# Kernel optimization log

Measured on AMD Instinct MI355X. Metric: run time of the kernel, lower is better.

## Reference

```python
import jax, jax.numpy as jnp
import numpy as np

B, C, D, T = 64, 512, 32, 32
DT = D * T
K = 128            # valid_num: top-K proposals kept for NMS-style pooling
MARGIN = 0.2       # opt.global_margin
MAX_VIOLATION = True
EPS = 1e-8         # torch.cosine_similarity eps


def _l2n(x, axis):
    # torch cosine_similarity normalizes each vector by max(||x||, eps)
    return x / jnp.maximum(jnp.linalg.norm(x, axis=axis, keepdims=True), EPS)


def _cos(a, b, axis):
    return jnp.sum(_l2n(a, axis) * _l2n(b, axis), axis=axis)


def setup_inputs() -> dict:
    key = jax.random.key(0)
    k1, k2, k3 = jax.random.split(key, 3)
    videos = jax.random.normal(k1, (B, C, D, T), jnp.float32)
    sentences = jax.random.normal(k2, (B, C), jnp.float32)
    iou = jax.random.uniform(k3, (DT, DT), jnp.float32)
    iou_maps = 0.5 * (iou + iou.T)
    iou_maps = iou_maps.at[jnp.arange(DT), jnp.arange(DT)].set(1.0)
    mask = jnp.ones((D, T), jnp.float32)
    lam = jnp.asarray(0.125, jnp.float32)
    return {"videos": videos, "sentences": sentences, "lam": lam,
            "mask": mask, "valid_num": K, "iou_maps": iou_maps}


def reference(videos, sentences, lam, mask, valid_num, iou_maps):
    b, c, d, t = videos.shape
    dt = d * t
    # center over channel dim (dim=1 in torch)
    V = videos - jnp.mean(videos, axis=1, keepdims=True)          # [b,c,d,t]
    S = sentences - jnp.mean(sentences, axis=1, keepdims=True)    # [b,c]
    Vf = V.reshape(b, c, dt)
    Vn = _l2n(Vf, axis=1)                                         # unit over c
    Sn = _l2n(S, axis=1)
    mflat = mask.reshape(dt)

    # cosine sim of every sentence vs every video proposal: [b_sent, b_vid, dt]
    cross = jnp.einsum('ic,jcp->ijp', Sn, Vn)
    cross = jnp.where(mflat == 0, -jnp.inf, cross)

    # --- per-sample positive pooling (loop 1) ---
    self_score = cross[jnp.arange(b), jnp.arange(b)]              # [b, dt]
    w = jax.nn.softmax(self_score, axis=-1)
    video_pos = jnp.einsum('bp,bcp->bc', w, Vf)                   # [b, c]

    # sentence-sentence sims + hard negative mining
    sim = Sn @ Sn.T                                               # [b, b]
    idx = jnp.argsort(-sim, axis=1)                               # descending
    neg_idx = idx[:, 6:b - 5]                                     # b > 11 path
    neg_sents = S[neg_idx]                                        # [b, b-11, c]
    pos_score = _cos(video_pos, S, axis=1)                        # [b]
    neg_score = _cos(video_pos[:, None, :], neg_sents, axis=2)    # [b, b-11]
    vas_loss = jnp.mean(jax.nn.relu(MARGIN + neg_score - pos_score[:, None]), axis=1).mean()

    # cross-video pseudo-positive (crov), gated on nearest-neighbor sim > 0.9
    nn_idx = idx[:, 1]
    pse = Vf[nn_idx]                                              # [b, c, dt]
    vsim = jax.nn.softmax(_cos(video_pos[:, :, None], pse, axis=1), axis=-1)  # [b, dt]
    p_v = jnp.einsum('bp,bcp->bc', vsim, pse)
    n_v = jnp.einsum('bp,bcp->bc', (1.0 - vsim) * mflat, pse) / (valid_num - 1)
    crov = jax.nn.relu(MARGIN + _cos(video_pos, n_v, axis=1) - _cos(video_pos, p_v, axis=1))
    gate = sim[jnp.arange(b), nn_idx] > 0.9
    crov_loss = jnp.where(gate, crov, 0.0).mean()

    # --- NMS-weighted video score pooling (loop 2) ---
    pmap = self_score.reshape(b, d, t)                            # postive_map
    topv, topi = jax.lax.top_k(cross, valid_num)                  # [b,b,K]
    # pairwise IoU among the top-K proposals of each (sentence, video) pair
    iou = iou_maps[topi[..., :, None], topi[..., None, :]]        # [b,b,K,K]
    lower = jnp.tril(jnp.ones((valid_num, valid_num), bool), -1)  # l < k
    decay = jnp.prod(1.0 - jnp.where(lower, iou, 0.0), axis=-1)   # [b,b,K]
    wk = jax.nn.softmax(lam * topv, axis=-1)
    scores = jnp.sum(wk * decay * topv, axis=-1)                  # [b,b]

    # bidirectional margin ranking loss
    diag = jnp.diag(scores)[:, None]
    eye = jnp.eye(b, dtype=bool)
    cost_s = jnp.where(eye, 0.0, jax.nn.relu(MARGIN + scores - diag))
    cost_im = jnp.where(eye, 0.0, jax.nn.relu(MARGIN + scores - diag.T))
    if MAX_VIOLATION:
        cost_s = cost_s.max(axis=1)
        cost_im = cost_im.max(axis=0)
    loss = cost_s.sum() / b + cost_im.sum() / b + vas_loss + crov_loss
    return loss, pmap
```

## Files before the change

kernel.cpp:

```cpp
#include <hip/hip_runtime.h>
#include <hip/hip_fp16.h>
#include <math.h>

#define BB 64
#define CC 512
#define DTT 1024
#define NNEG 53
#define MARGIN_ 0.2f
#define EPSV 1e-8f
#define KC 32

__device__ __forceinline__ float bred_sum(float v, float* red, int tid, int nt) {
  red[tid] = v; __syncthreads();
  for (int s = nt >> 1; s > 0; s >>= 1) { if (tid < s) red[tid] += red[tid + s]; __syncthreads(); }
  float r = red[0]; __syncthreads();
  return r;
}
__device__ __forceinline__ float bred_max(float v, float* red, int tid, int nt) {
  red[tid] = v; __syncthreads();
  for (int s = nt >> 1; s > 0; s >>= 1) { if (tid < s) red[tid] = fmaxf(red[tid], red[tid + s]); __syncthreads(); }
  float r = red[0]; __syncthreads();
  return r;
}

__global__ void k_sent(const float* __restrict__ sent, float* __restrict__ Sn,
                       float* __restrict__ SnT, float* __restrict__ SnSum) {
  int b = blockIdx.x, tid = threadIdx.x;
  __shared__ float red[256];
  float x0 = sent[b * CC + tid], x1 = sent[b * CC + tid + 256];
  float mean = bred_sum(x0 + x1, red, tid, 256) * (1.0f / CC);
  float s0 = x0 - mean, s1 = x1 - mean;
  float ss = bred_sum(s0 * s0 + s1 * s1, red, tid, 256);
  float nrm = fmaxf(sqrtf(ss), EPSV);
  float n0 = s0 / nrm, n1 = s1 / nrm;
  Sn[b * CC + tid] = n0; Sn[b * CC + tid + 256] = n1;
  SnT[tid * BB + b] = n0; SnT[(tid + 256) * BB + b] = n1;
  float sn = bred_sum(n0 + n1, red, tid, 256);
  if (tid == 0) SnSum[b] = sn;
}

__global__ void k_sim(const float* __restrict__ Sn, int* __restrict__ nn_idx,
                      int* __restrict__ negidx, float* __restrict__ nnsim) {
  int i = blockIdx.x, j = threadIdx.x;
  float dot = 0.f;
  for (int c = 0; c < CC; ++c) dot += Sn[i * CC + c] * Sn[j * CC + c];
  __shared__ float srow[BB];
  srow[j] = dot; __syncthreads();
  float mv = srow[j];
  int rank = 0;
  for (int k = 0; k < BB; ++k) {
    float vk = srow[k];
    if (vk > mv || (vk == mv && k < j)) rank++;
  }
  if (rank == 1) { nn_idx[i] = j; nnsim[i] = mv; }
  if (rank >= 6 && rank < 59) negidx[i * NNEG + rank - 6] = j;
}

__global__ void k_prep_iou(const float* __restrict__ iou, __half* __restrict__ L16) {
  int g = (blockIdx.x * 256 + threadIdx.x) * 4;
  float4 x = *(const float4*)(iou + g);
  __half2 h0 = __floats2half2_rn(1.f - x.x, 1.f - x.y);
  __half2 h1 = __floats2half2_rn(1.f - x.z, 1.f - x.w);
  *(__half2*)(L16 + g) = h0;
  *(__half2*)(L16 + g + 2) = h1;
}

__global__ __launch_bounds__(256) void k_cross(const float* __restrict__ videos,
    const float* __restrict__ SnT, const float* __restrict__ SnSum,
    const float* __restrict__ mask, float* __restrict__ cross,
    float* __restrict__ meanv, float* __restrict__ normv) {
  __shared__ float As[KC][68];
  __shared__ float Bs[KC][132];
  __shared__ float Smb[128], Sinv[128];
  int tid = threadIdx.x;
  int j = blockIdx.x >> 3;
  int p0 = (blockIdx.x & 7) << 7;
  int px = tid & 31;
  int iy = tid >> 5;
  int r = tid >> 3;
  int ca = (tid & 7) * 8;
  int cb = (tid & 7) * 16;
  const float* vrow = videos + (size_t)j * CC * DTT + p0 + cb;
  const float* arow0 = SnT + r * BB + ca;

  float acc[8][4];
#pragma unroll
  for (int a = 0; a < 8; ++a)
#pragma unroll
    for (int q = 0; q < 4; ++q) acc[a][q] = 0.f;
  float s4[4] = {0.f, 0.f, 0.f, 0.f}, ss4[4] = {0.f, 0.f, 0.f, 0.f};

  float4 a0 = *(const float4*)(arow0);
  float4 a1 = *(const float4*)(arow0 + 4);
  const float* vr0 = vrow + (size_t)r * DTT;
  float4 b0 = *(const float4*)(vr0);
  float4 b1 = *(const float4*)(vr0 + 4);
  float4 b2 = *(const float4*)(vr0 + 8);
  float4 b3 = *(const float4*)(vr0 + 12);

  for (int kc = 0; kc < CC; kc += KC) {
    *(float4*)&As[r][ca] = a0; *(float4*)&As[r][ca + 4] = a1;
    *(float4*)&Bs[r][cb] = b0; *(float4*)&Bs[r][cb + 4] = b1;
    *(float4*)&Bs[r][cb + 8] = b2; *(float4*)&Bs[r][cb + 12] = b3;
    __syncthreads();
    if (kc + KC < CC) {
      const float* ar = SnT + (size_t)(kc + KC + r) * BB + ca;
      a0 = *(const float4*)(ar); a1 = *(const float4*)(ar + 4);
      const float* vr = vrow + (size_t)(kc + KC + r) * DTT;
      b0 = *(const float4*)(vr); b1 = *(const float4*)(vr + 4);
      b2 = *(const float4*)(vr + 8); b3 = *(const float4*)(vr + 12);
    }
#pragma unroll
    for (int kk = 0; kk < KC; ++kk) {
      float bq[4], ai[8];
      *(float4*)&bq[0] = *(const float4*)&Bs[kk][px * 4];
      *(float4*)&ai[0] = *(const float4*)&As[kk][iy * 8];
      *(float4*)&ai[4] = *(const float4*)&As[kk][iy * 8 + 4];
      if (iy == 0) {
#pragma unroll
        for (int q = 0; q < 4; ++q) { s4[q] += bq[q]; ss4[q] = fmaf(bq[q], bq[q], ss4[q]); }
      }
#pragma unroll
      for (int a = 0; a < 8; ++a)
#pragma unroll
        for (int q = 0; q < 4; ++q)
          acc[a][q] = fmaf(ai[a], bq[q], acc[a][q]);
    }
    __syncthreads();
  }

  if (iy == 0) {
#pragma unroll
    for (int q = 0; q < 4; ++q) {
      float mb = s4[q] * (1.0f / CC);
      float var = ss4[q] - s4[q] * mb;
      float nrm = fmaxf(sqrtf(fmaxf(var, 0.f)), EPSV);
      meanv[j * DTT + p0 + px * 4 + q] = mb;
      normv[j * DTT + p0 + px * 4 + q] = nrm;
      Smb[px * 4 + q] = mb;
      Sinv[px * 4 + q] = 1.f / nrm;
    }
  }
  __syncthreads();
  float mb[4], inv[4], mk[4];
#pragma unroll
  for (int q = 0; q < 4; ++q) {
    mb[q] = Smb[px * 4 + q];
    inv[q] = Sinv[px * 4 + q];
    mk[q] = mask[p0 + px * 4 + q];
  }
#pragma unroll
  for (int a = 0; a < 8; ++a) {
    int i = iy * 8 + a;
    float sni = SnSum[i];
    float4 outv;
    float tmp[4];
#pragma unroll
    for (int q = 0; q < 4; ++q) {
      float val = (acc[a][q] - mb[q] * sni) * inv[q];
      tmp[q] = (mk[q] == 0.f) ? -INFINITY : val;
    }
    outv.x = tmp[0]; outv.y = tmp[1]; outv.z = tmp[2]; outv.w = tmp[3];
    *(float4*)(cross + ((size_t)i * BB + j) * DTT + p0 + px * 4) = outv;
  }
}

__global__ void k_softmax_w(const float* __restrict__ cross, const float* __restrict__ meanv,
                            float* __restrict__ pmap, float* __restrict__ w, float* __restrict__ wm) {
  int b = blockIdx.x, tid = threadIdx.x;
  __shared__ float red[256];
  const float* row = cross + ((size_t)b * BB + b) * DTT;
  float v[4]; float mx = -INFINITY;
#pragma unroll
  for (int q = 0; q < 4; ++q) {
    v[q] = row[q * 256 + tid];
    pmap[b * DTT + q * 256 + tid] = v[q];
    mx = fmaxf(mx, v[q]);
  }
  mx = bred_max(mx, red, tid, 256);
  float e[4]; float se = 0.f;
#pragma unroll
  for (int q = 0; q < 4; ++q) { e[q] = expf(v[q] - mx); se += e[q]; }
  se = bred_sum(se, red, tid, 256);
  float inv = 1.f / se;
  float wmacc = 0.f;
#pragma unroll
  for (int q = 0; q < 4; ++q) {
    float wv = e[q] * inv;
    w[b * DTT + q * 256 + tid] = wv;
    wmacc += wv * meanv[b * DTT + q * 256 + tid];
  }
  wmacc = bred_sum(wmacc, red, tid, 256);
  if (tid == 0) wm[b] = wmacc;
}

__global__ void k_vpos(const float* __restrict__ videos, const float* __restrict__ w,
                       const float* __restrict__ wm, float* __restrict__ vp) {
  int wid = (blockIdx.x * 256 + threadIdx.x) >> 6;
  int lane = threadIdx.x & 63;
  int b = wid >> 9, c = wid & 511;
  const float4* vb = (const float4*)(videos + (size_t)(b * CC + c) * DTT) + lane * 4;
  const float4* wb = (const float4*)(w + b * DTT) + lane * 4;
  float acc = 0.f;
#pragma unroll
  for (int q = 0; q < 4; ++q) {
    float4 x = vb[q], y = wb[q];
    acc += x.x * y.x + x.y * y.y + x.z * y.z + x.w * y.w;
  }
#pragma unroll
  for (int off = 32; off > 0; off >>= 1) acc += __shfl_xor(acc, off);
  if (lane == 0) vp[b * CC + c] = acc - wm[b];
}

__global__ void k_vpnorm(const float* __restrict__ vp, float* __restrict__ vpn,
                         float* __restrict__ vpsum) {
  int b = blockIdx.x, tid = threadIdx.x;
  __shared__ float red[256];
  float x0 = vp[b * CC + tid], x1 = vp[b * CC + tid + 256];
  float ss = bred_sum(x0 * x0 + x1 * x1, red, tid, 256);
  float sm = bred_sum(x0 + x1, red, tid, 256);
  if (tid == 0) { vpn[b] = fmaxf(sqrtf(ss), EPSV); vpsum[b] = sm; }
}

__global__ void k_vsim_logits(const float* __restrict__ videos, const float* __restrict__ vp,
    const float* __restrict__ vpn, const float* __restrict__ vpsum, const int* __restrict__ nn_idx,
    const float* __restrict__ meanv, const float* __restrict__ normv, float* __restrict__ vslog) {
  int gid = blockIdx.x * 256 + threadIdx.x;
  int b = gid >> 10, p = gid & 1023;
  int nn = nn_idx[b];
  const float* base = videos + (size_t)nn * CC * DTT + p;
  const float* vpr = vp + b * CC;
  float acc = 0.f;
#pragma unroll 8
  for (int c = 0; c < CC; ++c) acc = fmaf(vpr[c], base[(size_t)c * DTT], acc);
  acc -= meanv[nn * DTT + p] * vpsum[b];
  vslog[gid] = acc / (vpn[b] * normv[nn * DTT + p]);
}

__global__ void k_softmax_vsim(float* __restrict__ vslog, const int* __restrict__ nn_idx,
    const float* __restrict__ meanv, const float* __restrict__ mask,
    float* __restrict__ svp, float* __restrict__ svn) {
  int b = blockIdx.x, tid = threadIdx.x;
  __shared__ float red[256];
  int nn = nn_idx[b];
  float v[4]; float mx = -INFINITY;
#pragma unroll
  for (int q = 0; q < 4; ++q) { v[q] = vslog[b * DTT + q * 256 + tid]; mx = fmaxf(mx, v[q]); }
  mx = bred_max(mx, red, tid, 256);
  float e[4]; float se = 0.f;
#pragma unroll
  for (int q = 0; q < 4; ++q) { e[q] = expf(v[q] - mx); se += e[q]; }
  se = bred_sum(se, red, tid, 256);
  float inv = 1.f / se;
  float sp = 0.f, sn2 = 0.f;
#pragma unroll
  for (int q = 0; q < 4; ++q) {
    int p = q * 256 + tid;
    float vs = e[q] * inv;
    vslog[b * DTT + p] = vs;
    float mm = meanv[nn * DTT + p];
    sp += vs * mm;
    sn2 += (1.f - vs) * mask[p] * mm;
  }
  sp = bred_sum(sp, red, tid, 256);
  sn2 = bred_sum(sn2, red, tid, 256);
  if (tid == 0) { svp[b] = sp; svn[b] = sn2; }
}

__global__ void k_pvnv(const float* __restrict__ videos, const float* __restrict__ vsim,
    const int* __restrict__ nn_idx, const float* __restrict__ mask,
    const float* __restrict__ svp, const float* __restrict__ svn, const int* __restrict__ vn_p,
    float* __restrict__ pv, float* __restrict__ nv) {
  int wid = (blockIdx.x * 256 + threadIdx.x) >> 6;
  int lane = threadIdx.x & 63;
  int b = wid >> 9, c = wid & 511;
  int nn = nn_idx[b];
  const float4* vb = (const float4*)(videos + (size_t)(nn * CC + c) * DTT) + lane * 4;
  const float4* vs4 = (const float4*)(vsim + b * DTT) + lane * 4;
  const float4* m4 = ((const float4*)mask) + lane * 4;
  float ap = 0.f, an = 0.f;
#pragma unroll
  for (int q = 0; q < 4; ++q) {
    float4 x = vb[q], s = vs4[q], m = m4[q];
    ap += x.x * s.x + x.y * s.y + x.z * s.z + x.w * s.w;
    an += x.x * (1.f - s.x) * m.x + x.y * (1.f - s.y) * m.y + x.z * (1.f - s.z) * m.z + x.w * (1.f - s.w) * m.w;
  }
#pragma unroll
  for (int off = 32; off > 0; off >>= 1) { ap += __shfl_xor(ap, off); an += __shfl_xor(an, off); }
  if (lane == 0) {
    float kd = (float)(*vn_p - 1);
    pv[b * CC + c] = ap - svp[b];
    nv[b * CC + c] = (an - svn[b]) / kd;
  }
}

__global__ void k_vas(const float* __restrict__ vp, const float* __restrict__ vpn,
                      const float* __restrict__ Sn, const int* __restrict__ negidx,
                      float* __restrict__ vasrow) {
  int i = blockIdx.x, tid = threadIdx.x;
  __shared__ float red[64];
  __shared__ float pos;
  float invn = 1.f / vpn[i];
  float val = 0.f;
  if (tid < NNEG) {
    int nj = negidx[i * NNEG + tid];
    float d = 0.f;
    for (int c = 0; c < CC; ++c) d += vp[i * CC + c] * Sn[nj * CC + c];
    val = d * invn;
  }
  if (tid == 63) {
    float d = 0.f;
    for (int c = 0; c < CC; ++c) d += vp[i * CC + c] * Sn[i * CC + c];
    pos = d * invn;
  }
  __syncthreads();
  float contrib = (tid < NNEG) ? fmaxf(MARGIN_ + val - pos, 0.f) : 0.f;
  float s = bred_sum(contrib, red, tid, 64);
  if (tid == 0) vasrow[i] = s / (float)NNEG;
}

__global__ void k_crov(const float* __restrict__ vp, const float* __restrict__ vpn,
                       const float* __restrict__ pv, const float* __restrict__ nv,
                       const float* __restrict__ nnsim, float* __restrict__ crovrow) {
  int b = blockIdx.x, tid = threadIdx.x;
  __shared__ float red[256];
  float dp = 0.f, pp = 0.f, dn = 0.f, nn2 = 0.f;
  for (int c = tid; c < CC; c += 256) {
    float a = vp[b * CC + c], x = pv[b * CC + c], y = nv[b * CC + c];
    dp += a * x; pp += x * x; dn += a * y; nn2 += y * y;
  }
  dp = bred_sum(dp, red, tid, 256);
  pp = bred_sum(pp, red, tid, 256);
  dn = bred_sum(dn, red, tid, 256);
  nn2 = bred_sum(nn2, red, tid, 256);
  if (tid == 0) {
    float cosp = dp / (vpn[b] * fmaxf(sqrtf(pp), EPSV));
    float cosn = dn / (vpn[b] * fmaxf(sqrtf(nn2), EPSV));
    float crov = fmaxf(MARGIN_ + cosn - cosp, 0.f);
    crovrow[b] = (nnsim[b] > 0.9f) ? crov : 0.f;
  }
}

__global__ __launch_bounds__(256) void k_select(const float* __restrict__ cross,
    const int* __restrict__ vn_p, unsigned* __restrict__ ordi_g, float* __restrict__ ordv_g) {
  __shared__ unsigned int hist_s[4][256];
  __shared__ unsigned int sel_s[4][128];
  __shared__ unsigned int selk_s[4][128];
  __shared__ unsigned int cnt_s[4];
  int tid = threadIdx.x;
  int wv = tid >> 6, lane = tid & 63;
  int ij = blockIdx.x * 4 + wv;
  int K = *vn_p; if (K > 128) K = 128;
  unsigned int* hist = hist_s[wv];
  unsigned int* sel = sel_s[wv];
  unsigned int* selk = selk_s[wv];

  const float* row = cross + (size_t)ij * DTT;
  unsigned int v[16];
#pragma unroll
  for (int q = 0; q < 16; ++q) {
    unsigned u = __float_as_uint(row[q * 64 + lane]);
    v[q] = (u & 0x80000000u) ? ~u : (u | 0x80000000u);
  }
  if (lane == 0) cnt_s[wv] = 0u;
  __builtin_amdgcn_wave_barrier();

  unsigned prefix = 0u, pmask = 0u;
  int remaining = K;
  for (int shift = 24; shift >= 0; shift -= 8) {
#pragma unroll
    for (int q = 0; q < 4; ++q) hist[lane * 4 + q] = 0u;
    __builtin_amdgcn_wave_barrier();
#pragma unroll
    for (int q = 0; q < 16; ++q) {
      if ((v[q] & pmask) == prefix)
        atomicAdd(&hist[(v[q] >> shift) & 255u], 1u);
    }
    __builtin_amdgcn_wave_barrier();
    unsigned c0 = hist[lane * 4], c1 = hist[lane * 4 + 1];
    unsigned c2 = hist[lane * 4 + 2], c3 = hist[lane * 4 + 3];
    unsigned s = c0 + c1 + c2 + c3;
    unsigned inc = s;
#pragma unroll
    for (int off = 1; off < 64; off <<= 1) {
      unsigned t = __shfl_down(inc, off);
      if (lane + off < 64) inc += t;
    }
    unsigned exc = inc - s;
    bool found = (exc < (unsigned)remaining) && (inc >= (unsigned)remaining);
    unsigned long long bmask = __ballot(found);
    int winner = (int)(__ffsll((unsigned long long)bmask) - 1);
    unsigned packed = 0u;
    if (found) {
      unsigned c = exc;
      unsigned cc[4] = {c0, c1, c2, c3};
      int d = lane * 4;
#pragma unroll
      for (int q = 3; q >= 0; --q) {
        if (c + cc[q] >= (unsigned)remaining) { d = lane * 4 + q; break; }
        c += cc[q];
      }
      packed = ((unsigned)d << 16) | (unsigned)(remaining - (int)c);
    }
    packed = __shfl(packed, winner);
    prefix |= (packed >> 16) << shift;
    remaining = (int)(packed & 0xFFFFu);
    pmask |= 255u << shift;
  }

#pragma unroll
  for (int q = 0; q < 16; ++q) {
    if (v[q] > prefix) {
      unsigned pos = atomicAdd(&cnt_s[wv], 1u);
      sel[pos] = (unsigned)(q * 64 + lane);
      selk[pos] = v[q];
    }
  }
  __builtin_amdgcn_wave_barrier();
  {
    int base = K - remaining;
    int last = -1;
    for (int t = 0; t < remaining; ++t) {
      int mymin = 0x7FFFFFFF;
#pragma unroll
      for (int q = 0; q < 16; ++q) {
        int idx = q * 64 + lane;
        if (v[q] == prefix && idx > last && idx < mymin) mymin = idx;
      }
#pragma unroll
      for (int off = 32; off > 0; off >>= 1) mymin = min(mymin, __shfl_xor(mymin, off));
      if (lane == 0) { sel[base + t] = (unsigned)mymin; selk[base + t] = prefix; }
      last = mymin;
    }
  }
  __builtin_amdgcn_wave_barrier();

  for (int e = lane; e < K; e += 64) {
    unsigned myidx = sel[e], myk = selk[e];
    int rank = 0;
    for (int m = 0; m < K; ++m) {
      unsigned ok = selk[m];
      rank += (ok > myk || (ok == myk && sel[m] < myidx)) ? 1 : 0;
    }
    unsigned u = (myk & 0x80000000u) ? (myk & 0x7FFFFFFFu) : ~myk;
    ordi_g[ij * 128 + rank] = myidx;
    ordv_g[ij * 128 + rank] = __uint_as_float(u);
  }
}

__global__ __launch_bounds__(256) void k_decay(const __half* __restrict__ L16,
    const unsigned* __restrict__ ordi_g, const float* __restrict__ ordv_g,
    const float* __restrict__ lam_p, const int* __restrict__ vn_p,
    float* __restrict__ scores) {
  __shared__ unsigned ti[128];
  __shared__ float dks[128];
  int ij = blockIdx.x, tid = threadIdx.x;
  int wv = tid >> 6, lane = tid & 63;
  int K = *vn_p; if (K > 128) K = 128;
  float lam = *lam_p;
  if (tid < 128) {
    ti[tid] = (tid < K) ? ordi_g[ij * 128 + tid] : 0u;
    dks[tid] = 1.f;
  }
  __syncthreads();

  for (int r = wv; r < K; r += 4) {
    const __half* irow = L16 + (size_t)ti[r] * DTT;
    float f = 1.f;
    if (lane < r && lane < 64) f = __half2float(irow[ti[lane]]);
    float prod = f;
#pragma unroll
    for (int off = 32; off > 0; off >>= 1) prod *= __shfl_xor(prod, off);
    if (r > 64 && prod > 1e-14f) {
      float f2 = 1.f;
      int m = 64 + lane;
      if (m < r) f2 = __half2float(irow[ti[m]]);
#pragma unroll
      for (int off = 32; off > 0; off >>= 1) f2 *= __shfl_xor(f2, off);
      prod *= f2;
    }
    if (lane == 0) dks[r] = prod;
  }
  __syncthreads();

  if (wv == 0) {
    bool okA = (lane < K), okB = (lane + 64 < K);
    float vA = okA ? ordv_g[ij * 128 + lane] : 0.f;
    float vB = okB ? ordv_g[ij * 128 + lane + 64] : 0.f;
    float mx = fmaxf(okA ? lam * vA : -INFINITY, okB ? lam * vB : -INFINITY);
#pragma unroll
    for (int off = 32; off > 0; off >>= 1) mx = fmaxf(mx, __shfl_xor(mx, off));
    float eA = okA ? expf(lam * vA - mx) : 0.f;
    float eB = okB ? expf(lam * vB - mx) : 0.f;
    float se = eA + eB;
    float sc = (okA ? eA * dks[lane] * vA : 0.f) + (okB ? eB * dks[lane + 64] * vB : 0.f);
#pragma unroll
    for (int off = 32; off > 0; off >>= 1) {
      se += __shfl_xor(se, off);
      sc += __shfl_xor(sc, off);
    }
    if (lane == 0) scores[ij] = sc / se;
  }
}

__global__ void k_final(const float* __restrict__ scores, const float* __restrict__ vasrow,
                        const float* __restrict__ crovrow, float* __restrict__ out) {
  int tid = threadIdx.x;
  __shared__ float sm[BB * BB];
  __shared__ float red[64];
  for (int q = tid; q < BB * BB; q += 64) sm[q] = scores[q];
  __syncthreads();
  float di = sm[tid * BB + tid];
  float rowmax = 0.f, colmax = 0.f;
  for (int k = 0; k < BB; ++k) {
    if (k != tid) {
      rowmax = fmaxf(rowmax, fmaxf(MARGIN_ + sm[tid * BB + k] - di, 0.f));
      colmax = fmaxf(colmax, fmaxf(MARGIN_ + sm[k * BB + tid] - di, 0.f));
    }
  }
  float total = bred_sum(rowmax + colmax + vasrow[tid] + crovrow[tid], red, tid, 64);
  if (tid == 0) out[0] = total * (1.0f / BB);
}

extern "C" void kernel_launch(void* const* d_in, const int* in_sizes, int n_in,
                              void* d_out, int out_size, void* d_ws, size_t ws_size,
                              hipStream_t stream) {
  const float* videos = (const float*)d_in[0];
  const float* sentences = (const float*)d_in[1];
  const float* lam = (const float*)d_in[2];
  const float* mask = (const float*)d_in[3];
  const int* valid_num = (const int*)d_in[4];
  const float* iou_maps = (const float*)d_in[5];
  float* out = (float*)d_out;
  float* pmap = out + 1;

  float* ws = (float*)d_ws;
  float* Sn = ws;
  float* SnT = Sn + 32768;
  float* SnSum = SnT + 32768;
  float* meanv = SnSum + 64;
  float* normv = meanv + 65536;
  float* cross = normv + 65536;
  float* w = cross + 4194304;
  float* wm = w + 65536;
  float* vp = wm + 64;
  float* vpn = vp + 32768;
  float* vpsum = vpn + 64;
  float* nnsim = vpsum + 64;
  float* vslog = nnsim + 64;
  float* svp = vslog + 65536;
  float* svn = svp + 64;
  float* pvb = svn + 64;
  float* nvb = pvb + 32768;
  float* vasrow = nvb + 32768;
  float* crovrow = vasrow + 64;
  float* scores = crovrow + 64;
  int* nn_idx = (int*)(scores + 4096);
  int* negidx = nn_idx + 64;
  unsigned* ordi_g = (unsigned*)(negidx + 3392);
  float* ordv_g = (float*)(ordi_g + 524288);
  __half* L16 = (__half*)(ordv_g + 524288);

  k_sent<<<64, 256, 0, stream>>>(sentences, Sn, SnT, SnSum);
  k_sim<<<64, 64, 0, stream>>>(Sn, nn_idx, negidx, nnsim);
  k_prep_iou<<<1024, 256, 0, stream>>>(iou_maps, L16);
  k_cross<<<512, 256, 0, stream>>>(videos, SnT, SnSum, mask, cross, meanv, normv);
  k_softmax_w<<<64, 256, 0, stream>>>(cross, meanv, pmap, w, wm);
  k_vpos<<<8192, 256, 0, stream>>>(videos, w, wm, vp);
  k_vpnorm<<<64, 256, 0, stream>>>(vp, vpn, vpsum);
  k_vsim_logits<<<256, 256, 0, stream>>>(videos, vp, vpn, vpsum, nn_idx, meanv, normv, vslog);
  k_softmax_vsim<<<64, 256, 0, stream>>>(vslog, nn_idx, meanv, mask, svp, svn);
  k_pvnv<<<8192, 256, 0, stream>>>(videos, vslog, nn_idx, mask, svp, svn, valid_num, pvb, nvb);
  k_vas<<<64, 64, 0, stream>>>(vp, vpn, Sn, negidx, vasrow);
  k_crov<<<64, 256, 0, stream>>>(vp, vpn, pvb, nvb, nnsim, crovrow);
  k_select<<<1024, 256, 0, stream>>>(cross, valid_num, ordi_g, ordv_g);
  k_decay<<<4096, 256, 0, stream>>>(L16, ordi_g, ordv_g, lam, valid_num, scores);
  k_final<<<1, 64, 0, stream>>>(scores, vasrow, crovrow, out);
}
```

Before: 459.2 us.

## Compute cross similarity GEMM with split-bf16 MFMA instead of fp32 FMA

Replaces the scalar fp32 FMA tiled GEMM in k_cross with bf16 MFMA 16x16x32 instructions. It uses a three-term hi/lo bf16 split (hi*hi, hi*lo, lo*hi) so the products stay close to fp32 accuracy. Sentence vectors are pre-split into hi/lo bf16 arrays in k_sent, and video tiles are split on the fly into LDS. Channel mean and variance are reduced across threads through shared memory. This targets the FMA-bound GEMM but adds conversion work and a small precision change from the dropped lo*lo term.

```diff
diff --git a/kernel.cpp b/kernel.cpp
--- a/kernel.cpp
+++ b/kernel.cpp
@@ -8,7 +8,10 @@
 #define NNEG 53
 #define MARGIN_ 0.2f
 #define EPSV 1e-8f
-#define KC 32
+#define LDB 132
+
+typedef short s16x8 __attribute__((ext_vector_type(8)));
+typedef float f32x4 __attribute__((ext_vector_type(4)));
 
 __device__ __forceinline__ float bred_sum(float v, float* red, int tid, int nt) {
   red[tid] = v; __syncthreads();
@@ -24,7 +27,8 @@
 }
 
 __global__ void k_sent(const float* __restrict__ sent, float* __restrict__ Sn,
-                       float* __restrict__ SnT, float* __restrict__ SnSum) {
+                       unsigned short* __restrict__ SnH, unsigned short* __restrict__ SnL,
+                       float* __restrict__ SnSum) {
   int b = blockIdx.x, tid = threadIdx.x;
   __shared__ float red[256];
   float x0 = sent[b * CC + tid], x1 = sent[b * CC + tid + 256];
@@ -34,7 +38,13 @@
   float nrm = fmaxf(sqrtf(ss), EPSV);
   float n0 = s0 / nrm, n1 = s1 / nrm;
   Sn[b * CC + tid] = n0; Sn[b * CC + tid + 256] = n1;
-  SnT[tid * BB + b] = n0; SnT[(tid + 256) * BB + b] = n1;
+  unsigned u0 = __float_as_uint(n0), u1 = __float_as_uint(n1);
+  SnH[b * CC + tid] = (unsigned short)(u0 >> 16);
+  SnH[b * CC + tid + 256] = (unsigned short)(u1 >> 16);
+  float l0 = n0 - __uint_as_float(u0 & 0xFFFF0000u);
+  float l1 = n1 - __uint_as_float(u1 & 0xFFFF0000u);
+  SnL[b * CC + tid] = (unsigned short)(__float_as_uint(l0) >> 16);
+  SnL[b * CC + tid + 256] = (unsigned short)(__float_as_uint(l1) >> 16);
   float sn = bred_sum(n0 + n1, red, tid, 256);
   if (tid == 0) SnSum[b] = sn;
 }
@@ -66,102 +76,139 @@
 }
 
 __global__ __launch_bounds__(256) void k_cross(const float* __restrict__ videos,
-    const float* __restrict__ SnT, const float* __restrict__ SnSum,
-    const float* __restrict__ mask, float* __restrict__ cross,
-    float* __restrict__ meanv, float* __restrict__ normv) {
-  __shared__ float As[KC][68];
-  __shared__ float Bs[KC][132];
-  __shared__ float Smb[128], Sinv[128];
+    const unsigned short* __restrict__ SnH, const unsigned short* __restrict__ SnL,
+    const float* __restrict__ SnSum, const float* __restrict__ mask,
+    float* __restrict__ cross, float* __restrict__ meanv, float* __restrict__ normv) {
+  __shared__ unsigned int BH[16][LDB];
+  __shared__ unsigned int BL[16][LDB];
+  __shared__ float SnSum_s[64];
+  __shared__ float mb_s[128];
+  __shared__ float inv_s[128];
+
   int tid = threadIdx.x;
   int j = blockIdx.x >> 3;
   int p0 = (blockIdx.x & 7) << 7;
-  int px = tid & 31;
-  int iy = tid >> 5;
-  int r = tid >> 3;
-  int ca = (tid & 7) * 8;
-  int cb = (tid & 7) * 16;
-  const float* vrow = videos + (size_t)j * CC * DTT + p0 + cb;
-  const float* arow0 = SnT + r * BB + ca;
-
-  float acc[8][4];
-#pragma unroll
-  for (int a = 0; a < 8; ++a)
-#pragma unroll
-    for (int q = 0; q < 4; ++q) acc[a][q] = 0.f;
-  float s4[4] = {0.f, 0.f, 0.f, 0.f}, ss4[4] = {0.f, 0.f, 0.f, 0.f};
-
-  float4 a0 = *(const float4*)(arow0);
-  float4 a1 = *(const float4*)(arow0 + 4);
-  const float* vr0 = vrow + (size_t)r * DTT;
-  float4 b0 = *(const float4*)(vr0);
-  float4 b1 = *(const float4*)(vr0 + 4);
-  float4 b2 = *(const float4*)(vr0 + 8);
-  float4 b3 = *(const float4*)(vr0 + 12);
-
-  for (int kc = 0; kc < CC; kc += KC) {
-    *(float4*)&As[r][ca] = a0; *(float4*)&As[r][ca + 4] = a1;
-    *(float4*)&Bs[r][cb] = b0; *(float4*)&Bs[r][cb + 4] = b1;
-    *(float4*)&Bs[r][cb + 8] = b2; *(float4*)&Bs[r][cb + 12] = b3;
+  int lane = tid & 63;
+  int wv = tid >> 6;
+  int row = lane & 15;
+  int g = lane >> 4;
+  int g8 = g << 3;
+  int pA = wv << 5;
+
+  int kp = tid >> 4;
+  int pb = (tid & 15) << 3;
+
+  const float* vbase = videos + ((size_t)j * CC) * DTT + p0;
+
+  f32x4 acc[4][2];
+#pragma unroll
+  for (int a = 0; a < 4; ++a)
+#pragma unroll
+    for (int pf = 0; pf < 2; ++pf)
+#pragma unroll
+      for (int r = 0; r < 4; ++r) acc[a][pf][r] = 0.f;
+
+  float sacc[8], ssacc[8];
+#pragma unroll
+  for (int q = 0; q < 8; ++q) { sacc[q] = 0.f; ssacc[q] = 0.f; }
+
+  const float* pr = vbase + (size_t)(2 * kp) * DTT + pb;
+  float4 f0 = *(const float4*)(pr);
+  float4 f1 = *(const float4*)(pr + 4);
+  float4 f2 = *(const float4*)(pr + DTT);
+  float4 f3 = *(const float4*)(pr + DTT + 4);
+
+  for (int kc = 0; kc < CC; kc += 32) {
+    s16x8 AH[4], AL[4];
+#pragma unroll
+    for (int a = 0; a < 4; ++a) {
+      int off = (a * 16 + row) * CC + kc + g8;
+      AH[a] = *(const s16x8*)(SnH + off);
+      AL[a] = *(const s16x8*)(SnL + off);
+    }
+    {
+      float xe[8] = {f0.x, f0.y, f0.z, f0.w, f1.x, f1.y, f1.z, f1.w};
+      float xo[8] = {f2.x, f2.y, f2.z, f2.w, f3.x, f3.y, f3.z, f3.w};
+      unsigned int hw[8], lw[8];
+#pragma unroll
+      for (int q = 0; q < 8; ++q) {
+        unsigned ue = __float_as_uint(xe[q]);
+        unsigned uo = __float_as_uint(xo[q]);
+        hw[q] = (ue >> 16) | (uo & 0xFFFF0000u);
+        float el = xe[q] - __uint_as_float(ue & 0xFFFF0000u);
+        float ol = xo[q] - __uint_as_float(uo & 0xFFFF0000u);
+        lw[q] = (__float_as_uint(el) >> 16) | (__float_as_uint(ol) & 0xFFFF0000u);
+        sacc[q] += xe[q] + xo[q];
+        ssacc[q] = fmaf(xe[q], xe[q], ssacc[q]);
+        ssacc[q] = fmaf(xo[q], xo[q], ssacc[q]);
+      }
+      *(uint4*)&BH[kp][pb]     = make_uint4(hw[0], hw[1], hw[2], hw[3]);
+      *(uint4*)&BH[kp][pb + 4] = make_uint4(hw[4], hw[5], hw[6], hw[7]);
+      *(uint4*)&BL[kp][pb]     = make_uint4(lw[0], lw[1], lw[2], lw[3]);
+      *(uint4*)&BL[kp][pb + 4] = make_uint4(lw[4], lw[5], lw[6], lw[7]);
+    }
+    if (kc + 32 < CC) {
+      const float* pn = vbase + (size_t)(kc + 32 + 2 * kp) * DTT + pb;
+      f0 = *(const float4*)(pn);
+      f1 = *(const float4*)(pn + 4);
+      f2 = *(const float4*)(pn + DTT);
+      f3 = *(const float4*)(pn + DTT + 4);
+    }
     __syncthreads();
-    if (kc + KC < CC) {
-      const float* ar = SnT + (size_t)(kc + KC + r) * BB + ca;
-      a0 = *(const float4*)(ar); a1 = *(const float4*)(ar + 4);
-      const float* vr = vrow + (size_t)(kc + KC + r) * DTT;
-      b0 = *(const float4*)(vr); b1 = *(const float4*)(vr + 4);
-      b2 = *(const float4*)(vr + 8); b3 = *(const float4*)(vr + 12);
-    }
-#pragma unroll
-    for (int kk = 0; kk < KC; ++kk) {
-      float bq[4], ai[8];
-      *(float4*)&bq[0] = *(const float4*)&Bs[kk][px * 4];
-      *(float4*)&ai[0] = *(const float4*)&As[kk][iy * 8];
-      *(float4*)&ai[4] = *(const float4*)&As[kk][iy * 8 + 4];
-      if (iy == 0) {
-#pragma unroll
-        for (int q = 0; q < 4; ++q) { s4[q] += bq[q]; ss4[q] = fmaf(bq[q], bq[q], ss4[q]); }
+#pragma unroll
+    for (int pf = 0; pf < 2; ++pf) {
+      int p = pA + pf * 16 + row;
+      int kpb = g << 2;
+      union { unsigned int u[4]; s16x8 v; } bh, bl;
+      bh.u[0] = BH[kpb][p]; bh.u[1] = BH[kpb + 1][p];
+      bh.u[2] = BH[kpb + 2][p]; bh.u[3] = BH[kpb + 3][p];
+      bl.u[0] = BL[kpb][p]; bl.u[1] = BL[kpb + 1][p];
+      bl.u[2] = BL[kpb + 2][p]; bl.u[3] = BL[kpb + 3][p];
+#pragma unroll
+      for (int a = 0; a < 4; ++a) {
+        acc[a][pf] = __builtin_amdgcn_mfma_f32_16x16x32_bf16(AH[a], bh.v, acc[a][pf], 0, 0, 0);
+        acc[a][pf] = __builtin_amdgcn_mfma_f32_16x16x32_bf16(AH[a], bl.v, acc[a][pf], 0, 0, 0);
+        acc[a][pf] = __builtin_amdgcn_mfma_f32_16x16x32_bf16(AL[a], bh.v, acc[a][pf], 0, 0, 0);
       }
-#pragma unroll
-      for (int a = 0; a < 8; ++a)
-#pragma unroll
-        for (int q = 0; q < 4; ++q)
-          acc[a][q] = fmaf(ai[a], bq[q], acc[a][q]);
     }
     __syncthreads();
   }
 
-  if (iy == 0) {
-#pragma unroll
-    for (int q = 0; q < 4; ++q) {
-      float mb = s4[q] * (1.0f / CC);
-      float var = ss4[q] - s4[q] * mb;
-      float nrm = fmaxf(sqrtf(fmaxf(var, 0.f)), EPSV);
-      meanv[j * DTT + p0 + px * 4 + q] = mb;
-      normv[j * DTT + p0 + px * 4 + q] = nrm;
-      Smb[px * 4 + q] = mb;
-      Sinv[px * 4 + q] = 1.f / nrm;
-    }
-  }
+  float (*Sred)[LDB] = (float(*)[LDB])BH;
+  float (*SSred)[LDB] = (float(*)[LDB])BL;
+#pragma unroll
+  for (int q = 0; q < 8; ++q) { Sred[kp][pb + q] = sacc[q]; SSred[kp][pb + q] = ssacc[q]; }
+  if (tid < 64) SnSum_s[tid] = SnSum[tid];
   __syncthreads();
-  float mb[4], inv[4], mk[4];
-#pragma unroll
-  for (int q = 0; q < 4; ++q) {
-    mb[q] = Smb[px * 4 + q];
-    inv[q] = Sinv[px * 4 + q];
-    mk[q] = mask[p0 + px * 4 + q];
-  }
-#pragma unroll
-  for (int a = 0; a < 8; ++a) {
-    int i = iy * 8 + a;
-    float sni = SnSum[i];
-    float4 outv;
-    float tmp[4];
-#pragma unroll
-    for (int q = 0; q < 4; ++q) {
-      float val = (acc[a][q] - mb[q] * sni) * inv[q];
-      tmp[q] = (mk[q] == 0.f) ? -INFINITY : val;
-    }
-    outv.x = tmp[0]; outv.y = tmp[1]; outv.z = tmp[2]; outv.w = tmp[3];
-    *(float4*)(cross + ((size_t)i * BB + j) * DTT + p0 + px * 4) = outv;
+  if (tid < 128) {
+    float s = 0.f, ss = 0.f;
+#pragma unroll
+    for (int k = 0; k < 16; ++k) { s += Sred[k][tid]; ss += SSred[k][tid]; }
+    float mb = s * (1.0f / CC);
+    float var = ss - s * mb;
+    float nrm = fmaxf(sqrtf(fmaxf(var, 0.f)), EPSV);
+    meanv[j * DTT + p0 + tid] = mb;
+    normv[j * DTT + p0 + tid] = nrm;
+    mb_s[tid] = mb;
+    inv_s[tid] = 1.f / nrm;
+  }
+  __syncthreads();
+
+#pragma unroll
+  for (int pf = 0; pf < 2; ++pf) {
+    int p = pA + pf * 16 + row;
+    float mb = mb_s[p], inv = inv_s[p];
+    float mk = mask[p0 + p];
+#pragma unroll
+    for (int a = 0; a < 4; ++a) {
+#pragma unroll
+      for (int r = 0; r < 4; ++r) {
+        int i = a * 16 + (g << 2) + r;
+        float val = (acc[a][pf][r] - mb * SnSum_s[i]) * inv;
+        if (mk == 0.f) val = -INFINITY;
+        cross[((size_t)i * BB + j) * DTT + p0 + p] = val;
+      }
+    }
   }
 }
 
@@ -536,8 +583,8 @@
 
   float* ws = (float*)d_ws;
   float* Sn = ws;
-  float* SnT = Sn + 32768;
-  float* SnSum = SnT + 32768;
+  float* SnT_unused = Sn + 32768;
+  float* SnSum = SnT_unused + 32768;
   float* meanv = SnSum + 64;
   float* normv = meanv + 65536;
   float* cross = normv + 65536;
@@ -560,11 +607,13 @@
   unsigned* ordi_g = (unsigned*)(negidx + 3392);
   float* ordv_g = (float*)(ordi_g + 524288);
   __half* L16 = (__half*)(ordv_g + 524288);
-
-  k_sent<<<64, 256, 0, stream>>>(sentences, Sn, SnT, SnSum);
+  unsigned short* SnH16 = (unsigned short*)(L16 + 1048576);
+  unsigned short* SnL16 = SnH16 + 32768;
+
+  k_sent<<<64, 256, 0, stream>>>(sentences, Sn, SnH16, SnL16, SnSum);
   k_sim<<<64, 64, 0, stream>>>(Sn, nn_idx, negidx, nnsim);
   k_prep_iou<<<1024, 256, 0, stream>>>(iou_maps, L16);
-  k_cross<<<512, 256, 0, stream>>>(videos, SnT, SnSum, mask, cross, meanv, normv);
+  k_cross<<<512, 256, 0, stream>>>(videos, SnH16, SnL16, SnSum, mask, cross, meanv, normv);
   k_softmax_w<<<64, 256, 0, stream>>>(cross, meanv, pmap, w, wm);
   k_vpos<<<8192, 256, 0, stream>>>(videos, w, wm, vp);
   k_vpnorm<<<64, 256, 0, stream>>>(vp, vpn, vpsum);
```

Result: faster. 433.1 us (-5.7%).
